# Optimization experiments

Hardware: AMD Instinct MI355X
Metric: run time of the kernel (lower is better)

Reference implementation:

```python
import jax, jax.numpy as jnp
import numpy as np

GROUPS = 8
NUM_HEADS = 4
EPS = 1e-5

def setup_inputs() -> dict:
    key = jax.random.key(0)
    k1, k2, k3 = jax.random.split(key, 3)
    B, C, H, W = 4, 128, 64, 64
    x = jax.random.normal(k1, (B, C, H, W), dtype=jnp.float32)
    gn_w = jnp.ones((C,), jnp.float32)
    gn_b = jnp.zeros((C,), jnp.float32)
    qkv_w = jax.random.normal(k2, (3 * C, C), dtype=jnp.float32) * (1.0 / np.sqrt(C))
    qkv_b = jnp.zeros((3 * C,), jnp.float32)
    proj_w = jax.random.normal(k3, (C, C), dtype=jnp.float32) * (1.0 / np.sqrt(C))
    proj_b = jnp.zeros((C,), jnp.float32)
    return {"x": x, "gn_w": gn_w, "gn_b": gn_b, "qkv_w": qkv_w,
            "qkv_b": qkv_b, "proj_w": proj_w, "proj_b": proj_b}

def group_norm(x, w, b):
    B, C, H, W = x.shape
    xg = x.reshape(B, GROUPS, C // GROUPS, H, W)
    mean = jnp.mean(xg, axis=(2, 3, 4), keepdims=True)
    var = jnp.var(xg, axis=(2, 3, 4), keepdims=True)
    xn = ((xg - mean) * jax.lax.rsqrt(var + EPS)).reshape(B, C, H, W)
    return xn * w[None, :, None, None] + b[None, :, None, None]

def reference(x, gn_w, gn_b, qkv_w, qkv_b, proj_w, proj_b):
    B, C, H, W = x.shape
    nh = NUM_HEADS
    hd = C // nh
    xn = group_norm(x, gn_w, gn_b)  # residual is the NORMALIZED x (torch code reassigns x)
    # 1x1 conv == channel matmul
    qkv = jnp.einsum('oc,bchw->bohw', qkv_w, xn) + qkv_b[None, :, None, None]
    qkv = qkv.reshape(B, 3, nh, hd, H * W)
    q, k, v = qkv[:, 0], qkv[:, 1], qkv[:, 2]          # [B, nh, hd, HW]
    attn = jnp.einsum('bhcd,bhce->bhde', q, k) * (C ** -0.5)  # note: full-C scale, as in torch code
    attn = jax.nn.softmax(attn, axis=-1)
    out = jnp.einsum('bhde,bhce->bhcd', attn, v).reshape(B, C, H, W)
    out = jnp.einsum('oc,bchw->bohw', proj_w, out) + proj_b[None, :, None, None]
    return out + xn
```

## Files before the change

### kernel.cpp

```cpp
#include <hip/hip_runtime.h>
#include <math.h>

#define BATCH 4
#define C 128
#define HW 4096
#define G 8
#define CPG 16
#define NH 4
#define HD 32
#define EPS 1e-5f
#define SCALE 0.08838834764831845f
#define LOG2E 1.44269504088896340f
#define KP 40
#define GP 136

typedef unsigned int uint;
typedef unsigned short ushort;
typedef __attribute__((ext_vector_type(8))) short bf16x8;
typedef __attribute__((ext_vector_type(4))) float f32x4;

__device__ __forceinline__ ushort f2bf(float x) {
  uint u = __float_as_uint(x);
  u += 0x7fff + ((u >> 16) & 1);
  return (ushort)(u >> 16);
}
__device__ __forceinline__ ushort f2bf_r(float x) {
  return (ushort)((__float_as_uint(x) + 0x8000u) >> 16);
}
__device__ __forceinline__ float bf2f(ushort h) {
  return __uint_as_float(((uint)h) << 16);
}
__device__ __forceinline__ uint pk(float a, float b) {
#if __has_builtin(__builtin_amdgcn_cvt_pk_bf16_f32)
  auto r = __builtin_amdgcn_cvt_pk_bf16_f32(a, b);
  union { decltype(r) v; uint u; } x;
  x.v = r;
  return x.u;
#else
  uint ua = __float_as_uint(a) + 0x8000u;
  uint ub = __float_as_uint(b) + 0x8000u;
  return __builtin_amdgcn_perm(ub, ua, 0x07060302);
#endif
}
__device__ __forceinline__ bf16x8 as_bf(uint4 u) {
  union { uint4 a; bf16x8 b; } x; x.a = u; return x.b;
}
__device__ __forceinline__ float fexp2(float x) {
#if __has_builtin(__builtin_amdgcn_exp2f)
  return __builtin_amdgcn_exp2f(x);
#else
  return __exp2f(x);
#endif
}

__global__ __launch_bounds__(256) void gn_part(
    const float* __restrict__ x, float* __restrict__ stats) {
  const int bg = blockIdx.x >> 3, chunk = blockIdx.x & 7;
  const float* xp = x + (size_t)bg * (CPG * HW) + chunk * 8192;
  const int tid = threadIdx.x;
  float s = 0.f, ss = 0.f;
  #pragma unroll
  for (int j = 0; j < 8; j++) {
    float4 v = ((const float4*)xp)[j * 256 + tid];
    s += (v.x + v.y) + (v.z + v.w);
    ss += (v.x * v.x + v.y * v.y) + (v.z * v.z + v.w * v.w);
  }
  #pragma unroll
  for (int off = 32; off; off >>= 1) {
    s  += __shfl_down(s, off);
    ss += __shfl_down(ss, off);
  }
  __shared__ float rs[4], rss[4];
  const int lane = tid & 63, wid = tid >> 6;
  if (lane == 0) { rs[wid] = s; rss[wid] = ss; }
  __syncthreads();
  if (tid == 0) {
    stats[(bg * 8 + chunk) * 2]     = (rs[0] + rs[1]) + (rs[2] + rs[3]);
    stats[(bg * 8 + chunk) * 2 + 1] = (rss[0] + rss[1]) + (rss[2] + rss[3]);
  }
}

__global__ __launch_bounds__(256) void gn_apply(
    const float* __restrict__ x, const float* __restrict__ w,
    const float* __restrict__ b, const float* __restrict__ stats,
    ushort* __restrict__ xnb) {
  const int c = blockIdx.x, batch = blockIdx.y;
  const int bg = batch * G + (c >> 4);
  float s = 0.f, ss = 0.f;
  #pragma unroll
  for (int k = 0; k < 8; k++) {
    s  += stats[(bg * 8 + k) * 2];
    ss += stats[(bg * 8 + k) * 2 + 1];
  }
  const float mean = s * (1.0f / 65536.0f);
  const float var  = ss * (1.0f / 65536.0f) - mean * mean;
  const float inv  = rsqrtf(var + EPS);
  const float ca = w[c] * inv;
  const float cb = b[c] - mean * ca;
  const size_t base = ((size_t)batch * C + c) * HW;
  const float* xp = x + base;
  ushort* op = xnb + base;
  const int tid = threadIdx.x;
  #pragma unroll
  for (int j = 0; j < 4; j++) {
    int i = (j * 256 + tid) * 4;
    float4 v = *(const float4*)&xp[i];
    uint2 u;
    u.x = pk(fmaf(v.x, ca, cb), fmaf(v.y, ca, cb));
    u.y = pk(fmaf(v.z, ca, cb), fmaf(v.w, ca, cb));
    *(uint2*)&op[i] = u;
  }
}

__global__ __launch_bounds__(256) void qkv_gemm(
    const ushort* __restrict__ xnb, const float* __restrict__ w,
    const float* __restrict__ bias, ushort* __restrict__ qkvb) {
  const int b = blockIdx.z, m0 = blockIdx.y * 64, n0 = blockIdx.x * 64;
  const int tid = threadIdx.x, lane = tid & 63, wv = tid >> 6;
  const int li = lane & 15, g = lane >> 4;
  __shared__ ushort Ws[64][GP];
  __shared__ ushort Xs[64][GP];

  {
    const int row = tid >> 2, c0 = (tid & 3) * 32;
    const float* wr = w + (size_t)(m0 + row) * C + c0;
    #pragma unroll
    for (int k = 0; k < 4; k++) {
      float4 f0 = ((const float4*)wr)[k * 2];
      float4 f1 = ((const float4*)wr)[k * 2 + 1];
      uint4 u = {pk(f0.x, f0.y), pk(f0.z, f0.w), pk(f1.x, f1.y), pk(f1.z, f1.w)};
      *(uint4*)&Ws[row][c0 + k * 8] = u;
    }
  }
  {
    const int nX = tid & 63, c0 = (tid >> 6) * 32;
    const ushort* xb = xnb + (size_t)(b * C + c0) * HW + n0 + nX;
    #pragma unroll
    for (int k = 0; k < 4; k++) {
      ushort t8[8];
      #pragma unroll
      for (int j = 0; j < 8; j++) t8[j] = xb[(size_t)(k * 8 + j) * HW];
      uint4 u;
      u.x = t8[0] | ((uint)t8[1] << 16);
      u.y = t8[2] | ((uint)t8[3] << 16);
      u.z = t8[4] | ((uint)t8[5] << 16);
      u.w = t8[6] | ((uint)t8[7] << 16);
      *(uint4*)&Xs[nX][c0 + k * 8] = u;
    }
  }
  __syncthreads();

  f32x4 acc[4];
  #pragma unroll
  for (int nt = 0; nt < 4; nt++) acc[nt] = (f32x4){0.f, 0.f, 0.f, 0.f};
  #pragma unroll
  for (int kk = 0; kk < 4; kk++) {
    bf16x8 af = *(const bf16x8*)&Ws[wv * 16 + li][kk * 32 + g * 8];
    #pragma unroll
    for (int nt = 0; nt < 4; nt++) {
      bf16x8 bfr = *(const bf16x8*)&Xs[nt * 16 + li][kk * 32 + g * 8];
      acc[nt] = __builtin_amdgcn_mfma_f32_16x16x32_bf16(af, bfr, acc[nt], 0, 0, 0);
    }
  }
  const int ob = m0 + wv * 16 + g * 4;
  #pragma unroll
  for (int r = 0; r < 4; r++) {
    float bi = bias[ob + r];
    #pragma unroll
    for (int nt = 0; nt < 4; nt++) {
      qkvb[(size_t)(b * 3 * C + ob + r) * HW + n0 + nt * 16 + li] = f2bf(acc[nt][r] + bi);
    }
  }
}

__global__ __launch_bounds__(256) void kvprep_kernel(
    const ushort* __restrict__ qkvb, ushort* __restrict__ kt) {
  const int bh = blockIdx.y, b = bh >> 2, h = bh & 3;
  const int e0 = blockIdx.x * 64;
  const ushort* kp = qkvb + (size_t)(b * 3 * C + C + h * HD) * HW;
  ushort* ktp = kt + (size_t)bh * HW * HD;
  const int t = threadIdx.x;

  __shared__ ushort Kt[32][66];
  {
    const int c = t >> 3, e8 = (t & 7) * 8;
    *(uint4*)&Kt[c][e8] = *(const uint4*)&kp[(size_t)c * HW + e0 + e8];
  }
  __syncthreads();
  {
    const int e = t >> 2, c0 = (t & 3) * 8;
    ushort o[8];
    #pragma unroll
    for (int j = 0; j < 8; j++) o[j] = Kt[c0 + j][e];
    uint4 u;
    u.x = o[0] | ((uint)o[1] << 16);
    u.y = o[2] | ((uint)o[3] << 16);
    u.z = o[4] | ((uint)o[5] << 16);
    u.w = o[6] | ((uint)o[7] << 16);
    *(uint4*)&ktp[(size_t)(e0 + e) * HD + c0] = u;
  }
}

__global__ __launch_bounds__(512, 6) void attn_kernel(
    ushort* __restrict__ qkv, const ushort* __restrict__ kt) {
  const int bh = blockIdx.y, b = bh >> 2, h = bh & 3;
  const int tid = threadIdx.x, lane = tid & 63, wv = tid >> 6;
  const int li = lane & 15, g = lane >> 4;
  const int grp = wv >> 2, w4 = wv & 3;
  ushort* qp = qkv + (size_t)(b * 3 * C + h * HD) * HW;
  const ushort* vpl = qkv + (size_t)(b * 3 * C + 2 * C + h * HD) * HW;
  const ushort* ktp = kt + (size_t)bh * HW * HD;
  const int d0 = blockIdx.x * 128 + w4 * 32;

  struct SmemT {
    union {
      struct { ushort Ks[2][2][32][KP]; ushort Vs[2][2][32][KP]; } t;
      float OP[8][64][19];
    };
  };
  __shared__ SmemT sm;

  const float qs = SCALE * LOG2E;
  bf16x8 qf[2];
  #pragma unroll
  for (int dt = 0; dt < 2; dt++) {
    int d = d0 + dt * 16 + li;
    float qv[8];
    #pragma unroll
    for (int j = 0; j < 8; j++)
      qv[j] = bf2f(qp[(size_t)(g * 8 + j) * HW + d]) * qs;
    uint4 qu = {pk(qv[0], qv[1]), pk(qv[2], qv[3]), pk(qv[4], qv[5]), pk(qv[6], qv[7])};
    qf[dt] = as_bf(qu);
  }

  f32x4 O[2][2];
  #pragma unroll
  for (int dt = 0; dt < 2; dt++)
    #pragma unroll
    for (int ct = 0; ct < 2; ct++) O[dt][ct] = (f32x4){0.f, 0.f, 0.f, 0.f};
  f32x4 lacc[2] = {(f32x4){0.f, 0.f, 0.f, 0.f}, (f32x4){0.f, 0.f, 0.f, 0.f}};
  const uint one2 = 0x3F803F80u;
  const bf16x8 ones = as_bf((uint4){one2, one2, one2, one2});

  const int gt = tid & 255;
  const bool isK = gt < 128;
  const int t2 = gt & 127;
  const int srow = t2 >> 2, scol8 = (t2 & 3) * 8;
  const ushort* gK = ktp + (size_t)(grp * 64) * 1024 + t2 * 8;
  const ushort* gV = vpl + (size_t)srow * HW + grp * 2048 + scol8;

  uint4 st = isK ? *(const uint4*)&gK[0] : *(const uint4*)&gV[0];
  if (isK) *(uint4*)&sm.t.Ks[grp][0][srow][scol8] = st;
  else     *(uint4*)&sm.t.Vs[grp][0][srow][scol8] = st;
  st = isK ? *(const uint4*)&gK[1024] : *(const uint4*)&gV[32];
  __syncthreads();

  for (int it = 0; it < 64; it++) {
    const int cur = it & 1, nxt = cur ^ 1;
    if (isK) *(uint4*)&sm.t.Ks[grp][nxt][srow][scol8] = st;
    else     *(uint4*)&sm.t.Vs[grp][nxt][srow][scol8] = st;

    bf16x8 kf0 = *(const bf16x8*)&sm.t.Ks[grp][cur][li][g * 8];
    bf16x8 kf1 = *(const bf16x8*)&sm.t.Ks[grp][cur][16 + li][g * 8];
    uint2 va0 = *(const uint2*)&sm.t.Vs[grp][cur][li][4 * g];
    uint2 va1 = *(const uint2*)&sm.t.Vs[grp][cur][li][16 + 4 * g];
    uint2 vb0 = *(const uint2*)&sm.t.Vs[grp][cur][16 + li][4 * g];
    uint2 vb1 = *(const uint2*)&sm.t.Vs[grp][cur][16 + li][16 + 4 * g];
    bf16x8 vf0 = as_bf((uint4){va0.x, va0.y, va1.x, va1.y});
    bf16x8 vf1 = as_bf((uint4){vb0.x, vb0.y, vb1.x, vb1.y});

    const int tn = (it + 2) & 63;
    st = isK ? *(const uint4*)&gK[(size_t)tn * 1024] : *(const uint4*)&gV[tn * 32];

    const f32x4 z = (f32x4){0.f, 0.f, 0.f, 0.f};
    #pragma unroll
    for (int dt = 0; dt < 2; dt++) {
      f32x4 s0 = __builtin_amdgcn_mfma_f32_16x16x32_bf16(kf0, qf[dt], z, 0, 0, 0);
      f32x4 s1 = __builtin_amdgcn_mfma_f32_16x16x32_bf16(kf1, qf[dt], z, 0, 0, 0);
      float p0 = fexp2(s0[0]), p1 = fexp2(s0[1]), p2 = fexp2(s0[2]), p3 = fexp2(s0[3]);
      float p4 = fexp2(s1[0]), p5 = fexp2(s1[1]), p6 = fexp2(s1[2]), p7 = fexp2(s1[3]);
      uint4 pu = {pk(p0, p1), pk(p2, p3), pk(p4, p5), pk(p6, p7)};
      bf16x8 pf = as_bf(pu);
      lacc[dt] = __builtin_amdgcn_mfma_f32_16x16x32_bf16(ones, pf, lacc[dt], 0, 0, 0);
      O[dt][0] = __builtin_amdgcn_mfma_f32_16x16x32_bf16(vf0, pf, O[dt][0], 0, 0, 0);
      O[dt][1] = __builtin_amdgcn_mfma_f32_16x16x32_bf16(vf1, pf, O[dt][1], 0, 0, 0);
    }
    __syncthreads();
  }

  #pragma unroll
  for (int dt = 0; dt < 2; dt++) {
    #pragma unroll
    for (int ct = 0; ct < 2; ct++)
      #pragma unroll
      for (int r = 0; r < 4; r++) sm.OP[wv][lane][dt * 8 + ct * 4 + r] = O[dt][ct][r];
    sm.OP[wv][lane][16 + dt] = lacc[dt][0];
  }
  __syncthreads();
  const int pw = wv ^ 4;
  #pragma unroll
  for (int dt = 0; dt < 2; dt++) {
    const float inv = 1.0f / (lacc[dt][0] + sm.OP[pw][lane][16 + dt]);
    const int d = d0 + dt * 16 + li;
    #pragma unroll
    for (int r = 0; r < 4; r++) {
      float val = O[dt][grp][r] + sm.OP[pw][lane][dt * 8 + grp * 4 + r];
      qp[(size_t)(grp * 16 + g * 4 + r) * HW + d] = f2bf_r(val * inv);
    }
  }
}

__global__ __launch_bounds__(256) void proj_gemm(
    const ushort* __restrict__ qkvb, const float* __restrict__ w,
    const float* __restrict__ bias, const ushort* __restrict__ xnb, float* __restrict__ out) {
  const int b = blockIdx.z, m0 = blockIdx.y * 64, n0 = blockIdx.x * 64;
  const int tid = threadIdx.x, lane = tid & 63, wv = tid >> 6;
  const int li = lane & 15, g = lane >> 4;
  __shared__ ushort Ws[64][GP];
  __shared__ ushort Xs[64][GP];

  {
    const int row = tid >> 2, c0 = (tid & 3) * 32;
    const float* wr = w + (size_t)(m0 + row) * C + c0;
    #pragma unroll
    for (int k = 0; k < 4; k++) {
      float4 f0 = ((const float4*)wr)[k * 2];
      float4 f1 = ((const float4*)wr)[k * 2 + 1];
      uint4 u = {pk(f0.x, f0.y), pk(f0.z, f0.w), pk(f1.x, f1.y), pk(f1.z, f1.w)};
      *(uint4*)&Ws[row][c0 + k * 8] = u;
    }
  }
  {
    const int nX = tid & 63, c0 = (tid >> 6) * 32;
    const ushort* xb = qkvb + (size_t)(b * 3 * C + c0) * HW + n0 + nX;
    #pragma unroll
    for (int k = 0; k < 4; k++) {
      ushort t8[8];
      #pragma unroll
      for (int j = 0; j < 8; j++) t8[j] = xb[(size_t)(k * 8 + j) * HW];
      uint4 u;
      u.x = t8[0] | ((uint)t8[1] << 16);
      u.y = t8[2] | ((uint)t8[3] << 16);
      u.z = t8[4] | ((uint)t8[5] << 16);
      u.w = t8[6] | ((uint)t8[7] << 16);
      *(uint4*)&Xs[nX][c0 + k * 8] = u;
    }
  }
  __syncthreads();

  f32x4 acc[4];
  #pragma unroll
  for (int nt = 0; nt < 4; nt++) acc[nt] = (f32x4){0.f, 0.f, 0.f, 0.f};
  #pragma unroll
  for (int kk = 0; kk < 4; kk++) {
    bf16x8 af = *(const bf16x8*)&Ws[wv * 16 + li][kk * 32 + g * 8];
    #pragma unroll
    for (int nt = 0; nt < 4; nt++) {
      bf16x8 bfr = *(const bf16x8*)&Xs[nt * 16 + li][kk * 32 + g * 8];
      acc[nt] = __builtin_amdgcn_mfma_f32_16x16x32_bf16(af, bfr, acc[nt], 0, 0, 0);
    }
  }
  const int ob = m0 + wv * 16 + g * 4;
  #pragma unroll
  for (int r = 0; r < 4; r++) {
    float bi = bias[ob + r];
    #pragma unroll
    for (int nt = 0; nt < 4; nt++) {
      size_t idx = (size_t)(b * C + ob + r) * HW + n0 + nt * 16 + li;
      out[idx] = acc[nt][r] + bi + bf2f(xnb[idx]);
    }
  }
}

extern "C" void kernel_launch(void* const* d_in, const int* in_sizes, int n_in,
                              void* d_out, int out_size, void* d_ws, size_t ws_size,
                              hipStream_t stream) {
  const float* x     = (const float*)d_in[0];
  const float* gn_w  = (const float*)d_in[1];
  const float* gn_b  = (const float*)d_in[2];
  const float* qkv_w = (const float*)d_in[3];
  const float* qkv_b = (const float*)d_in[4];
  const float* pw    = (const float*)d_in[5];
  const float* pb    = (const float*)d_in[6];
  float* out = (float*)d_out;

  float*  stats = (float*)d_ws;
  ushort* xnb   = (ushort*)((char*)d_ws + 4096);
  ushort* qkvb  = xnb + (size_t)BATCH * C * HW;
  ushort* kt    = qkvb + (size_t)BATCH * 3 * C * HW;

  gn_part<<<dim3(256), dim3(256), 0, stream>>>(x, stats);
  gn_apply<<<dim3(C, BATCH), dim3(256), 0, stream>>>(x, gn_w, gn_b, stats, xnb);
  qkv_gemm<<<dim3(HW / 64, 6, BATCH), dim3(256), 0, stream>>>(xnb, qkv_w, qkv_b, qkvb);
  kvprep_kernel<<<dim3(HW / 64, BATCH * NH), dim3(256), 0, stream>>>(qkvb, kt);
  attn_kernel<<<dim3(HW / 128, BATCH * NH), dim3(512), 0, stream>>>(qkvb, kt);
  proj_gemm<<<dim3(HW / 64, 2, BATCH), dim3(256), 0, stream>>>(qkvb, pw, pb, xnb, out);
}
```

Before: 165.3 us.

## Fuse GroupNorm apply into QKV and projection GEMMs, drop bf16 normalized buffer

Removes the gn_apply kernel and its bf16 normalized-x buffer. The QKV GEMM now computes per-channel scale and shift from the group stats and normalizes fp32 x while staging it into shared memory. The projection GEMM recomputes the normalized residual from x in its epilogue. This saves a kernel launch and a full write and read of the intermediate, at the cost of reading fp32 x (twice the bytes) six times across the QKV m-tiles, plus redundant coefficient computation per block. Attention launch bounds also change from 6 to 4 minimum blocks.

```diff
diff --git a/kernel.cpp b/kernel.cpp
--- a/kernel.cpp
+++ b/kernel.cpp
@@ -80,11 +80,9 @@
   }
 }
 
-__global__ __launch_bounds__(256) void gn_apply(
-    const float* __restrict__ x, const float* __restrict__ w,
-    const float* __restrict__ b, const float* __restrict__ stats,
-    ushort* __restrict__ xnb) {
-  const int c = blockIdx.x, batch = blockIdx.y;
+__device__ __forceinline__ void gn_coeff(
+    const float* __restrict__ stats, const float* __restrict__ w,
+    const float* __restrict__ b, int batch, int c, float& ca, float& cb) {
   const int bg = batch * G + (c >> 4);
   float s = 0.f, ss = 0.f;
   #pragma unroll
@@ -95,31 +93,24 @@
   const float mean = s * (1.0f / 65536.0f);
   const float var  = ss * (1.0f / 65536.0f) - mean * mean;
   const float inv  = rsqrtf(var + EPS);
-  const float ca = w[c] * inv;
-  const float cb = b[c] - mean * ca;
-  const size_t base = ((size_t)batch * C + c) * HW;
-  const float* xp = x + base;
-  ushort* op = xnb + base;
-  const int tid = threadIdx.x;
-  #pragma unroll
-  for (int j = 0; j < 4; j++) {
-    int i = (j * 256 + tid) * 4;
-    float4 v = *(const float4*)&xp[i];
-    uint2 u;
-    u.x = pk(fmaf(v.x, ca, cb), fmaf(v.y, ca, cb));
-    u.y = pk(fmaf(v.z, ca, cb), fmaf(v.w, ca, cb));
-    *(uint2*)&op[i] = u;
-  }
+  ca = w[c] * inv;
+  cb = b[c] - mean * ca;
 }
 
 __global__ __launch_bounds__(256) void qkv_gemm(
-    const ushort* __restrict__ xnb, const float* __restrict__ w,
-    const float* __restrict__ bias, ushort* __restrict__ qkvb) {
+    const float* __restrict__ x, const float* __restrict__ stats,
+    const float* __restrict__ gnw, const float* __restrict__ gnb,
+    const float* __restrict__ w, const float* __restrict__ bias,
+    ushort* __restrict__ qkvb) {
   const int b = blockIdx.z, m0 = blockIdx.y * 64, n0 = blockIdx.x * 64;
   const int tid = threadIdx.x, lane = tid & 63, wv = tid >> 6;
   const int li = lane & 15, g = lane >> 4;
   __shared__ ushort Ws[64][GP];
   __shared__ ushort Xs[64][GP];
+  __shared__ float CA[C], CB[C];
+
+  if (tid < C) gn_coeff(stats, gnw, gnb, b, tid, CA[tid], CB[tid]);
+  __syncthreads();
 
   {
     const int row = tid >> 2, c0 = (tid & 3) * 32;
@@ -134,7 +125,209 @@
   }
   {
     const int nX = tid & 63, c0 = (tid >> 6) * 32;
-    const ushort* xb = xnb + (size_t)(b * C + c0) * HW + n0 + nX;
+    const float* xb = x + (size_t)(b * C + c0) * HW + n0 + nX;
+    #pragma unroll
+    for (int k = 0; k < 4; k++) {
+      float xv[8];
+      #pragma unroll
+      for (int j = 0; j < 8; j++) {
+        int c = c0 + k * 8 + j;
+        xv[j] = fmaf(xb[(size_t)(k * 8 + j) * HW], CA[c], CB[c]);
+      }
+      uint4 u = {pk(xv[0], xv[1]), pk(xv[2], xv[3]), pk(xv[4], xv[5]), pk(xv[6], xv[7])};
+      *(uint4*)&Xs[nX][c0 + k * 8] = u;
+    }
+  }
+  __syncthreads();
+
+  f32x4 acc[4];
+  #pragma unroll
+  for (int nt = 0; nt < 4; nt++) acc[nt] = (f32x4){0.f, 0.f, 0.f, 0.f};
+  #pragma unroll
+  for (int kk = 0; kk < 4; kk++) {
+    bf16x8 af = *(const bf16x8*)&Ws[wv * 16 + li][kk * 32 + g * 8];
+    #pragma unroll
+    for (int nt = 0; nt < 4; nt++) {
+      bf16x8 bfr = *(const bf16x8*)&Xs[nt * 16 + li][kk * 32 + g * 8];
+      acc[nt] = __builtin_amdgcn_mfma_f32_16x16x32_bf16(af, bfr, acc[nt], 0, 0, 0);
+    }
+  }
+  const int ob = m0 + wv * 16 + g * 4;
+  #pragma unroll
+  for (int r = 0; r < 4; r++) {
+    float bi = bias[ob + r];
+    #pragma unroll
+    for (int nt = 0; nt < 4; nt++) {
+      qkvb[(size_t)(b * 3 * C + ob + r) * HW + n0 + nt * 16 + li] = f2bf(acc[nt][r] + bi);
+    }
+  }
+}
+
+__global__ __launch_bounds__(256) void kvprep_kernel(
+    const ushort* __restrict__ qkvb, ushort* __restrict__ kt) {
+  const int bh = blockIdx.y, b = bh >> 2, h = bh & 3;
+  const int e0 = blockIdx.x * 64;
+  const ushort* kp = qkvb + (size_t)(b * 3 * C + C + h * HD) * HW;
+  ushort* ktp = kt + (size_t)bh * HW * HD;
+  const int t = threadIdx.x;
+
+  __shared__ ushort Kt[32][66];
+  {
+    const int c = t >> 3, e8 = (t & 7) * 8;
+    *(uint4*)&Kt[c][e8] = *(const uint4*)&kp[(size_t)c * HW + e0 + e8];
+  }
+  __syncthreads();
+  {
+    const int e = t >> 2, c0 = (t & 3) * 8;
+    ushort o[8];
+    #pragma unroll
+    for (int j = 0; j < 8; j++) o[j] = Kt[c0 + j][e];
+    uint4 u;
+    u.x = o[0] | ((uint)o[1] << 16);
+    u.y = o[2] | ((uint)o[3] << 16);
+    u.z = o[4] | ((uint)o[5] << 16);
+    u.w = o[6] | ((uint)o[7] << 16);
+    *(uint4*)&ktp[(size_t)(e0 + e) * HD + c0] = u;
+  }
+}
+
+__global__ __launch_bounds__(512, 4) void attn_kernel(
+    ushort* __restrict__ qkv, const ushort* __restrict__ kt) {
+  const int bh = blockIdx.y, b = bh >> 2, h = bh & 3;
+  const int tid = threadIdx.x, lane = tid & 63, wv = tid >> 6;
+  const int li = lane & 15, g = lane >> 4;
+  const int grp = wv >> 2, w4 = wv & 3;
+  ushort* qp = qkv + (size_t)(b * 3 * C + h * HD) * HW;
+  const ushort* vpl = qkv + (size_t)(b * 3 * C + 2 * C + h * HD) * HW;
+  const ushort* ktp = kt + (size_t)bh * HW * HD;
+  const int d0 = blockIdx.x * 128 + w4 * 32;
+
+  struct SmemT {
+    union {
+      struct { ushort Ks[2][2][32][KP]; ushort Vs[2][2][32][KP]; } t;
+      float OP[8][64][19];
+    };
+  };
+  __shared__ SmemT sm;
+
+  const float qs = SCALE * LOG2E;
+  bf16x8 qf[2];
+  #pragma unroll
+  for (int dt = 0; dt < 2; dt++) {
+    int d = d0 + dt * 16 + li;
+    float qv[8];
+    #pragma unroll
+    for (int j = 0; j < 8; j++)
+      qv[j] = bf2f(qp[(size_t)(g * 8 + j) * HW + d]) * qs;
+    uint4 qu = {pk(qv[0], qv[1]), pk(qv[2], qv[3]), pk(qv[4], qv[5]), pk(qv[6], qv[7])};
+    qf[dt] = as_bf(qu);
+  }
+
+  f32x4 O[2][2];
+  #pragma unroll
+  for (int dt = 0; dt < 2; dt++)
+    #pragma unroll
+    for (int ct = 0; ct < 2; ct++) O[dt][ct] = (f32x4){0.f, 0.f, 0.f, 0.f};
+  f32x4 lacc[2] = {(f32x4){0.f, 0.f, 0.f, 0.f}, (f32x4){0.f, 0.f, 0.f, 0.f}};
+  const uint one2 = 0x3F803F80u;
+  const bf16x8 ones = as_bf((uint4){one2, one2, one2, one2});
+
+  const int gt = tid & 255;
+  const bool isK = gt < 128;
+  const int t2 = gt & 127;
+  const int srow = t2 >> 2, scol8 = (t2 & 3) * 8;
+  const ushort* gK = ktp + (size_t)(grp * 64) * 1024 + t2 * 8;
+  const ushort* gV = vpl + (size_t)srow * HW + grp * 2048 + scol8;
+
+  uint4 st = isK ? *(const uint4*)&gK[0] : *(const uint4*)&gV[0];
+  if (isK) *(uint4*)&sm.t.Ks[grp][0][srow][scol8] = st;
+  else     *(uint4*)&sm.t.Vs[grp][0][srow][scol8] = st;
+  st = isK ? *(const uint4*)&gK[1024] : *(const uint4*)&gV[32];
+  __syncthreads();
+
+  for (int it = 0; it < 64; it++) {
+    const int cur = it & 1, nxt = cur ^ 1;
+    if (isK) *(uint4*)&sm.t.Ks[grp][nxt][srow][scol8] = st;
+    else     *(uint4*)&sm.t.Vs[grp][nxt][srow][scol8] = st;
+
+    bf16x8 kf0 = *(const bf16x8*)&sm.t.Ks[grp][cur][li][g * 8];
+    bf16x8 kf1 = *(const bf16x8*)&sm.t.Ks[grp][cur][16 + li][g * 8];
+    uint2 va0 = *(const uint2*)&sm.t.Vs[grp][cur][li][4 * g];
+    uint2 va1 = *(const uint2*)&sm.t.Vs[grp][cur][li][16 + 4 * g];
+    uint2 vb0 = *(const uint2*)&sm.t.Vs[grp][cur][16 + li][4 * g];
+    uint2 vb1 = *(const uint2*)&sm.t.Vs[grp][cur][16 + li][16 + 4 * g];
+    bf16x8 vf0 = as_bf((uint4){va0.x, va0.y, va1.x, va1.y});
+    bf16x8 vf1 = as_bf((uint4){vb0.x, vb0.y, vb1.x, vb1.y});
+
+    const int tn = (it + 2) & 63;
+    st = isK ? *(const uint4*)&gK[(size_t)tn * 1024] : *(const uint4*)&gV[tn * 32];
+
+    const f32x4 z = (f32x4){0.f, 0.f, 0.f, 0.f};
+    #pragma unroll
+    for (int dt = 0; dt < 2; dt++) {
+      f32x4 s0 = __builtin_amdgcn_mfma_f32_16x16x32_bf16(kf0, qf[dt], z, 0, 0, 0);
+      f32x4 s1 = __builtin_amdgcn_mfma_f32_16x16x32_bf16(kf1, qf[dt], z, 0, 0, 0);
+      float p0 = fexp2(s0[0]), p1 = fexp2(s0[1]), p2 = fexp2(s0[2]), p3 = fexp2(s0[3]);
+      float p4 = fexp2(s1[0]), p5 = fexp2(s1[1]), p6 = fexp2(s1[2]), p7 = fexp2(s1[3]);
+      uint4 pu = {pk(p0, p1), pk(p2, p3), pk(p4, p5), pk(p6, p7)};
+      bf16x8 pf = as_bf(pu);
+      lacc[dt] = __builtin_amdgcn_mfma_f32_16x16x32_bf16(ones, pf, lacc[dt], 0, 0, 0);
+      O[dt][0] = __builtin_amdgcn_mfma_f32_16x16x32_bf16(vf0, pf, O[dt][0], 0, 0, 0);
+      O[dt][1] = __builtin_amdgcn_mfma_f32_16x16x32_bf16(vf1, pf, O[dt][1], 0, 0, 0);
+    }
+    __syncthreads();
+  }
+
+  #pragma unroll
+  for (int dt = 0; dt < 2; dt++) {
+    #pragma unroll
+    for (int ct = 0; ct < 2; ct++)
+      #pragma unroll
+      for (int r = 0; r < 4; r++) sm.OP[wv][lane][dt * 8 + ct * 4 + r] = O[dt][ct][r];
+    sm.OP[wv][lane][16 + dt] = lacc[dt][0];
+  }
+  __syncthreads();
+  const int pw = wv ^ 4;
+  #pragma unroll
+  for (int dt = 0; dt < 2; dt++) {
+    const float inv = 1.0f / (lacc[dt][0] + sm.OP[pw][lane][16 + dt]);
+    const int d = d0 + dt * 16 + li;
+    #pragma unroll
+    for (int r = 0; r < 4; r++) {
+      float val = O[dt][grp][r] + sm.OP[pw][lane][dt * 8 + grp * 4 + r];
+      qp[(size_t)(grp * 16 + g * 4 + r) * HW + d] = f2bf_r(val * inv);
+    }
+  }
+}
+
+__global__ __launch_bounds__(256) void proj_gemm(
+    const ushort* __restrict__ qkvb, const float* __restrict__ w,
+    const float* __restrict__ bias, const float* __restrict__ x,
+    const float* __restrict__ stats, const float* __restrict__ gnw,
+    const float* __restrict__ gnb, float* __restrict__ out) {
+  const int b = blockIdx.z, m0 = blockIdx.y * 64, n0 = blockIdx.x * 64;
+  const int tid = threadIdx.x, lane = tid & 63, wv = tid >> 6;
+  const int li = lane & 15, g = lane >> 4;
+  __shared__ ushort Ws[64][GP];
+  __shared__ ushort Xs[64][GP];
+  __shared__ float CA[64], CB[64];
+
+  if (tid < 64) gn_coeff(stats, gnw, gnb, b, m0 + tid, CA[tid], CB[tid]);
+
+  {
+    const int row = tid >> 2, c0 = (tid & 3) * 32;
+    const float* wr = w + (size_t)(m0 + row) * C + c0;
+    #pragma unroll
+    for (int k = 0; k < 4; k++) {
+      float4 f0 = ((const float4*)wr)[k * 2];
+      float4 f1 = ((const float4*)wr)[k * 2 + 1];
+      uint4 u = {pk(f0.x, f0.y), pk(f0.z, f0.w), pk(f1.x, f1.y), pk(f1.z, f1.w)};
+      *(uint4*)&Ws[row][c0 + k * 8] = u;
+    }
+  }
+  {
+    const int nX = tid & 63, c0 = (tid >> 6) * 32;
+    const ushort* xb = qkvb + (size_t)(b * 3 * C + c0) * HW + n0 + nX;
     #pragma unroll
     for (int k = 0; k < 4; k++) {
       ushort t8[8];
@@ -165,209 +358,12 @@
   const int ob = m0 + wv * 16 + g * 4;
   #pragma unroll
   for (int r = 0; r < 4; r++) {
-    float bi = bias[ob + r];
-    #pragma unroll
-    for (int nt = 0; nt < 4; nt++) {
-      qkvb[(size_t)(b * 3 * C + ob + r) * HW + n0 + nt * 16 + li] = f2bf(acc[nt][r] + bi);
-    }
-  }
-}
-
-__global__ __launch_bounds__(256) void kvprep_kernel(
-    const ushort* __restrict__ qkvb, ushort* __restrict__ kt) {
-  const int bh = blockIdx.y, b = bh >> 2, h = bh & 3;
-  const int e0 = blockIdx.x * 64;
-  const ushort* kp = qkvb + (size_t)(b * 3 * C + C + h * HD) * HW;
-  ushort* ktp = kt + (size_t)bh * HW * HD;
-  const int t = threadIdx.x;
-
-  __shared__ ushort Kt[32][66];
-  {
-    const int c = t >> 3, e8 = (t & 7) * 8;
-    *(uint4*)&Kt[c][e8] = *(const uint4*)&kp[(size_t)c * HW + e0 + e8];
-  }
-  __syncthreads();
-  {
-    const int e = t >> 2, c0 = (t & 3) * 8;
-    ushort o[8];
-    #pragma unroll
-    for (int j = 0; j < 8; j++) o[j] = Kt[c0 + j][e];
-    uint4 u;
-    u.x = o[0] | ((uint)o[1] << 16);
-    u.y = o[2] | ((uint)o[3] << 16);
-    u.z = o[4] | ((uint)o[5] << 16);
-    u.w = o[6] | ((uint)o[7] << 16);
-    *(uint4*)&ktp[(size_t)(e0 + e) * HD + c0] = u;
-  }
-}
-
-__global__ __launch_bounds__(512, 6) void attn_kernel(
-    ushort* __restrict__ qkv, const ushort* __restrict__ kt) {
-  const int bh = blockIdx.y, b = bh >> 2, h = bh & 3;
-  const int tid = threadIdx.x, lane = tid & 63, wv = tid >> 6;
-  const int li = lane & 15, g = lane >> 4;
-  const int grp = wv >> 2, w4 = wv & 3;
-  ushort* qp = qkv + (size_t)(b * 3 * C + h * HD) * HW;
-  const ushort* vpl = qkv + (size_t)(b * 3 * C + 2 * C + h * HD) * HW;
-  const ushort* ktp = kt + (size_t)bh * HW * HD;
-  const int d0 = blockIdx.x * 128 + w4 * 32;
-
-  struct SmemT {
-    union {
-      struct { ushort Ks[2][2][32][KP]; ushort Vs[2][2][32][KP]; } t;
-      float OP[8][64][19];
-    };
-  };
-  __shared__ SmemT sm;
-
-  const float qs = SCALE * LOG2E;
-  bf16x8 qf[2];
-  #pragma unroll
-  for (int dt = 0; dt < 2; dt++) {
-    int d = d0 + dt * 16 + li;
-    float qv[8];
-    #pragma unroll
-    for (int j = 0; j < 8; j++)
-      qv[j] = bf2f(qp[(size_t)(g * 8 + j) * HW + d]) * qs;
-    uint4 qu = {pk(qv[0], qv[1]), pk(qv[2], qv[3]), pk(qv[4], qv[5]), pk(qv[6], qv[7])};
-    qf[dt] = as_bf(qu);
-  }
-
-  f32x4 O[2][2];
-  #pragma unroll
-  for (int dt = 0; dt < 2; dt++)
-    #pragma unroll
-    for (int ct = 0; ct < 2; ct++) O[dt][ct] = (f32x4){0.f, 0.f, 0.f, 0.f};
-  f32x4 lacc[2] = {(f32x4){0.f, 0.f, 0.f, 0.f}, (f32x4){0.f, 0.f, 0.f, 0.f}};
-  const uint one2 = 0x3F803F80u;
-  const bf16x8 ones = as_bf((uint4){one2, one2, one2, one2});
-
-  const int gt = tid & 255;
-  const bool isK = gt < 128;
-  const int t2 = gt & 127;
-  const int srow = t2 >> 2, scol8 = (t2 & 3) * 8;
-  const ushort* gK = ktp + (size_t)(grp * 64) * 1024 + t2 * 8;
-  const ushort* gV = vpl + (size_t)srow * HW + grp * 2048 + scol8;
-
-  uint4 st = isK ? *(const uint4*)&gK[0] : *(const uint4*)&gV[0];
-  if (isK) *(uint4*)&sm.t.Ks[grp][0][srow][scol8] = st;
-  else     *(uint4*)&sm.t.Vs[grp][0][srow][scol8] = st;
-  st = isK ? *(const uint4*)&gK[1024] : *(const uint4*)&gV[32];
-  __syncthreads();
-
-  for (int it = 0; it < 64; it++) {
-    const int cur = it & 1, nxt = cur ^ 1;
-    if (isK) *(uint4*)&sm.t.Ks[grp][nxt][srow][scol8] = st;
-    else     *(uint4*)&sm.t.Vs[grp][nxt][srow][scol8] = st;
-
-    bf16x8 kf0 = *(const bf16x8*)&sm.t.Ks[grp][cur][li][g * 8];
-    bf16x8 kf1 = *(const bf16x8*)&sm.t.Ks[grp][cur][16 + li][g * 8];
-    uint2 va0 = *(const uint2*)&sm.t.Vs[grp][cur][li][4 * g];
-    uint2 va1 = *(const uint2*)&sm.t.Vs[grp][cur][li][16 + 4 * g];
-    uint2 vb0 = *(const uint2*)&sm.t.Vs[grp][cur][16 + li][4 * g];
-    uint2 vb1 = *(const uint2*)&sm.t.Vs[grp][cur][16 + li][16 + 4 * g];
-    bf16x8 vf0 = as_bf((uint4){va0.x, va0.y, va1.x, va1.y});
-    bf16x8 vf1 = as_bf((uint4){vb0.x, vb0.y, vb1.x, vb1.y});
-
-    const int tn = (it + 2) & 63;
-    st = isK ? *(const uint4*)&gK[(size_t)tn * 1024] : *(const uint4*)&gV[tn * 32];
-
-    const f32x4 z = (f32x4){0.f, 0.f, 0.f, 0.f};
-    #pragma unroll
-    for (int dt = 0; dt < 2; dt++) {
-      f32x4 s0 = __builtin_amdgcn_mfma_f32_16x16x32_bf16(kf0, qf[dt], z, 0, 0, 0);
-      f32x4 s1 = __builtin_amdgcn_mfma_f32_16x16x32_bf16(kf1, qf[dt], z, 0, 0, 0);
-      float p0 = fexp2(s0[0]), p1 = fexp2(s0[1]), p2 = fexp2(s0[2]), p3 = fexp2(s0[3]);
-      float p4 = fexp2(s1[0]), p5 = fexp2(s1[1]), p6 = fexp2(s1[2]), p7 = fexp2(s1[3]);
-      uint4 pu = {pk(p0, p1), pk(p2, p3), pk(p4, p5), pk(p6, p7)};
-      bf16x8 pf = as_bf(pu);
-      lacc[dt] = __builtin_amdgcn_mfma_f32_16x16x32_bf16(ones, pf, lacc[dt], 0, 0, 0);
-      O[dt][0] = __builtin_amdgcn_mfma_f32_16x16x32_bf16(vf0, pf, O[dt][0], 0, 0, 0);
-      O[dt][1] = __builtin_amdgcn_mfma_f32_16x16x32_bf16(vf1, pf, O[dt][1], 0, 0, 0);
-    }
-    __syncthreads();
-  }
-
-  #pragma unroll
-  for (int dt = 0; dt < 2; dt++) {
-    #pragma unroll
-    for (int ct = 0; ct < 2; ct++)
-      #pragma unroll
-      for (int r = 0; r < 4; r++) sm.OP[wv][lane][dt * 8 + ct * 4 + r] = O[dt][ct][r];
-    sm.OP[wv][lane][16 + dt] = lacc[dt][0];
-  }
-  __syncthreads();
-  const int pw = wv ^ 4;
-  #pragma unroll
-  for (int dt = 0; dt < 2; dt++) {
-    const float inv = 1.0f / (lacc[dt][0] + sm.OP[pw][lane][16 + dt]);
-    const int d = d0 + dt * 16 + li;
-    #pragma unroll
-    for (int r = 0; r < 4; r++) {
-      float val = O[dt][grp][r] + sm.OP[pw][lane][dt * 8 + grp * 4 + r];
-      qp[(size_t)(grp * 16 + g * 4 + r) * HW + d] = f2bf_r(val * inv);
-    }
-  }
-}
-
-__global__ __launch_bounds__(256) void proj_gemm(
-    const ushort* __restrict__ qkvb, const float* __restrict__ w,
-    const float* __restrict__ bias, const ushort* __restrict__ xnb, float* __restrict__ out) {
-  const int b = blockIdx.z, m0 = blockIdx.y * 64, n0 = blockIdx.x * 64;
-  const int tid = threadIdx.x, lane = tid & 63, wv = tid >> 6;
-  const int li = lane & 15, g = lane >> 4;
-  __shared__ ushort Ws[64][GP];
-  __shared__ ushort Xs[64][GP];
-
-  {
-    const int row = tid >> 2, c0 = (tid & 3) * 32;
-    const float* wr = w + (size_t)(m0 + row) * C + c0;
-    #pragma unroll
-    for (int k = 0; k < 4; k++) {
-      float4 f0 = ((const float4*)wr)[k * 2];
-      float4 f1 = ((const float4*)wr)[k * 2 + 1];
-      uint4 u = {pk(f0.x, f0.y), pk(f0.z, f0.w), pk(f1.x, f1.y), pk(f1.z, f1.w)};
-      *(uint4*)&Ws[row][c0 + k * 8] = u;
-    }
-  }
-  {
-    const int nX = tid & 63, c0 = (tid >> 6) * 32;
-    const ushort* xb = qkvb + (size_t)(b * 3 * C + c0) * HW + n0 + nX;
-    #pragma unroll
-    for (int k = 0; k < 4; k++) {
-      ushort t8[8];
-      #pragma unroll
-      for (int j = 0; j < 8; j++) t8[j] = xb[(size_t)(k * 8 + j) * HW];
-      uint4 u;
-      u.x = t8[0] | ((uint)t8[1] << 16);
-      u.y = t8[2] | ((uint)t8[3] << 16);
-      u.z = t8[4] | ((uint)t8[5] << 16);
-      u.w = t8[6] | ((uint)t8[7] << 16);
-      *(uint4*)&Xs[nX][c0 + k * 8] = u;
-    }
-  }
-  __syncthreads();
-
-  f32x4 acc[4];
-  #pragma unroll
-  for (int nt = 0; nt < 4; nt++) acc[nt] = (f32x4){0.f, 0.f, 0.f, 0.f};
-  #pragma unroll
-  for (int kk = 0; kk < 4; kk++) {
-    bf16x8 af = *(const bf16x8*)&Ws[wv * 16 + li][kk * 32 + g * 8];
-    #pragma unroll
-    for (int nt = 0; nt < 4; nt++) {
-      bf16x8 bfr = *(const bf16x8*)&Xs[nt * 16 + li][kk * 32 + g * 8];
-      acc[nt] = __builtin_amdgcn_mfma_f32_16x16x32_bf16(af, bfr, acc[nt], 0, 0, 0);
-    }
-  }
-  const int ob = m0 + wv * 16 + g * 4;
-  #pragma unroll
-  for (int r = 0; r < 4; r++) {
-    float bi = bias[ob + r];
+    const float bi = bias[ob + r];
+    const float ca = CA[wv * 16 + g * 4 + r], cb = CB[wv * 16 + g * 4 + r];
     #pragma unroll
     for (int nt = 0; nt < 4; nt++) {
       size_t idx = (size_t)(b * C + ob + r) * HW + n0 + nt * 16 + li;
-      out[idx] = acc[nt][r] + bi + bf2f(xnb[idx]);
+      out[idx] = acc[nt][r] + bi + fmaf(x[idx], ca, cb);
     }
   }
 }
@@ -385,14 +381,14 @@
   float* out = (float*)d_out;
 
   float*  stats = (float*)d_ws;
-  ushort* xnb   = (ushort*)((char*)d_ws + 4096);
-  ushort* qkvb  = xnb + (size_t)BATCH * C * HW;
+  ushort* qkvb  = (ushort*)((char*)d_ws + 4096);
   ushort* kt    = qkvb + (size_t)BATCH * 3 * C * HW;
 
   gn_part<<<dim3(256), dim3(256), 0, stream>>>(x, stats);
-  gn_apply<<<dim3(C, BATCH), dim3(256), 0, stream>>>(x, gn_w, gn_b, stats, xnb);
-  qkv_gemm<<<dim3(HW / 64, 6, BATCH), dim3(256), 0, stream>>>(xnb, qkv_w, qkv_b, qkvb);
+  qkv_gemm<<<dim3(HW / 64, 6, BATCH), dim3(256), 0, stream>>>(
+      x, stats, gn_w, gn_b, qkv_w, qkv_b, qkvb);
   kvprep_kernel<<<dim3(HW / 64, BATCH * NH), dim3(256), 0, stream>>>(qkvb, kt);
   attn_kernel<<<dim3(HW / 128, BATCH * NH), dim3(512), 0, stream>>>(qkvb, kt);
-  proj_gemm<<<dim3(HW / 64, 2, BATCH), dim3(256), 0, stream>>>(qkvb, pw, pb, xnb, out);
-}
+  proj_gemm<<<dim3(HW / 64, 2, BATCH), dim3(256), 0, stream>>>(
+      qkvb, pw, pb, x, stats, gn_w, gn_b, out);
+}
```

After: 162.1 us. No clear change (-2.0%).
